# Optimization experiments

Hardware: AMD Instinct MI355X
Metric: run time of the kernel (lower is better)

Reference implementation:

```python
import jax, jax.numpy as jnp
import numpy as np

D_MODEL = 512
N_HEADS = 8
DH = D_MODEL // N_HEADS            # 64
Q_PROJ = D_MODEL // 2              # 256
KV_PROJ = (2 * D_MODEL) // 3       # 341
ROPE_DIM = D_MODEL // 8            # 64 total rope dims
R = ROPE_DIM // N_HEADS            # 8 rope dims per head
THETA = 10000.0
EPS = 1e-5
B, S = 2, 2048


def layernorm(x, g, b):
    m = jnp.mean(x, axis=-1, keepdims=True)
    v = jnp.var(x, axis=-1, keepdims=True)
    return (x - m) * jax.lax.rsqrt(v + EPS) * g + b


def rope_cos_sin(seq_len, dtype):
    inv_freq = THETA ** (-jnp.arange(0, R, 2, dtype=jnp.float32) / R)   # (R/2,)
    ang = jnp.arange(seq_len, dtype=jnp.float32)[:, None] * inv_freq   # (S, R/2)
    cos = jnp.concatenate([jnp.cos(ang), jnp.cos(ang)], axis=-1)        # (S, R)
    sin = jnp.concatenate([jnp.sin(ang), jnp.sin(ang)], axis=-1)
    return cos.astype(dtype), sin.astype(dtype)


def apply_rope(x, cos, sin):
    # x: (B, H, S, R); neox-style half rotation
    x1, x2 = jnp.split(x, 2, axis=-1)
    rot = jnp.concatenate([-x2, x1], axis=-1)
    return x * cos + rot * sin


def setup_inputs() -> dict:
    key = jax.random.key(0)
    ks = jax.random.split(key, 9)
    p = lambda k, shape: 0.01 * jax.random.normal(k, shape, jnp.float32)
    return {
        "x": jax.random.normal(ks[0], (B, S, D_MODEL), jnp.float32),
        "W_dq": p(ks[1], (D_MODEL, Q_PROJ)),
        "W_uq": p(ks[2], (Q_PROJ, D_MODEL)),
        "W_qr": p(ks[3], (Q_PROJ, ROPE_DIM)),
        "W_dkv": p(ks[4], (D_MODEL, KV_PROJ)),
        "W_ukv": p(ks[5], (KV_PROJ, 2 * D_MODEL)),
        "W_kr": p(ks[6], (D_MODEL, ROPE_DIM)),
        "W_o": p(ks[7], (D_MODEL, D_MODEL)),
        "q_ln_g": jnp.ones((Q_PROJ,), jnp.float32),
        "q_ln_b": jnp.zeros((Q_PROJ,), jnp.float32),
        "kv_ln_g": jnp.ones((KV_PROJ,), jnp.float32),
        "kv_ln_b": jnp.zeros((KV_PROJ,), jnp.float32),
    }


def reference(x, W_dq, W_uq, W_qr, W_dkv, W_ukv, W_kr, W_o,
              q_ln_g, q_ln_b, kv_ln_g, kv_ln_b):
    b, s, d = x.shape
    # --- low-rank Q path ---
    cq = layernorm(x @ W_dq, q_ln_g, q_ln_b)                      # (B,S,Q_PROJ)
    Q = (cq @ W_uq).reshape(b, s, N_HEADS, DH).transpose(0, 2, 1, 3)
    Qr = (cq @ W_qr).reshape(b, s, N_HEADS, R).transpose(0, 2, 1, 3)
    cos, sin = rope_cos_sin(s, x.dtype)
    Qr = apply_rope(Qr, cos, sin)
    q = jnp.concatenate([Q, Qr], axis=-1)                          # (B,H,S,DH+R)
    # --- low-rank KV path ---
    ckv = layernorm(x @ W_dkv, kv_ln_g, kv_ln_b)                  # (B,S,KV_PROJ)
    KV = ckv @ W_ukv                                              # (B,S,2*D)
    K, V = KV[..., :D_MODEL], KV[..., D_MODEL:]
    K = K.reshape(b, s, N_HEADS, DH).transpose(0, 2, 1, 3)
    Kr = (x @ W_kr).reshape(b, s, N_HEADS, R).transpose(0, 2, 1, 3)
    Kr = apply_rope(Kr, cos, sin)
    k = jnp.concatenate([K, Kr], axis=-1)                          # (B,H,S,DH+R)
    v = V.reshape(b, s, N_HEADS, DH).transpose(0, 2, 1, 3)         # (B,H,S,DH)
    # --- causal SDPA ---
    scale = 1.0 / jnp.sqrt(jnp.asarray(DH + R, x.dtype))
    scores = jnp.einsum('bhqd,bhkd->bhqk', q, k) * scale           # (B,H,S,S)
    mask = jnp.tril(jnp.ones((s, s), dtype=bool))
    scores = jnp.where(mask, scores, jnp.finfo(scores.dtype).min)
    attn = jax.nn.softmax(scores, axis=-1)
    out = jnp.einsum('bhqk,bhkd->bhqd', attn, v)
    out = out.transpose(0, 2, 1, 3).reshape(b, s, d)
    return out @ W_o.T, ckv
```

## Files before the change

### kernel.cpp

```cpp
#include <hip/hip_runtime.h>
#include <hip/hip_bf16.h>

#define BATCH 2
#define SEQ 2048
#define DM 512
#define NH 8
#define DHD 64
#define QP 256
#define KVP 341
#define DQKPAD 96
#define MROWS 4096

#define OFF_X     0
#define OFF_WDQ   2097152
#define OFF_WUQ   2228224
#define OFF_WQR   2359296
#define OFF_WDKV  2375680
#define OFF_WUKV  2550272
#define OFF_WKR   2899456
#define OFF_WO    2932224
#define OFF_QG    3194368
#define OFF_QB    3194624
#define OFF_KG    3194880
#define OFF_KB    3195221
#define N_ELEMS   3195562

#define T_DQ   0
#define T_DKV  131072
#define T_KR   327680
#define T_UQ   360448
#define T_QR   491520
#define T_UKV  507904
#define T_TOT  901120

typedef __bf16 bf16x8 __attribute__((ext_vector_type(8)));
typedef float f32x4 __attribute__((ext_vector_type(4)));
typedef __hip_bfloat16 bf16;
typedef unsigned short u16;

static __device__ __forceinline__ bf16x8 ld_bf8(const bf16* p) {
    return __builtin_bit_cast(bf16x8, *(const uint4*)p);
}

#define GL16(gp, lp) __builtin_amdgcn_global_load_lds( \
    (const __attribute__((address_space(1))) void*)(gp), \
    (__attribute__((address_space(3))) void*)(lp), 16, 0, 0)

__global__ void detect_k(const u16* __restrict__ x, int* __restrict__ flagp) {
    __shared__ int cnt;
    if (threadIdx.x == 0) cnt = 0;
    __syncthreads();
    int bad = 0;
    for (int i = threadIdx.x; i < 2048; i += 256) {
        u16 u = x[i];
        int e = (u >> 7) & 0xFF;
        if (u != 0 && (e < 90 || e > 164)) bad++;
    }
    atomicAdd(&cnt, bad);
    __syncthreads();
    if (threadIdx.x == 0) *flagp = (cnt > 256) ? 1 : 0;
}

__global__ __launch_bounds__(256) void cvt_all(
    const void* s0, const void* s1, const void* s2, const void* s3,
    const void* s4, const void* s5, const void* s6, const void* s7,
    const void* s8, const void* s9, const void* s10, const void* s11,
    u16* __restrict__ arena, const int* __restrict__ flagp)
{
    int gid = blockIdx.x * 256 + threadIdx.x;
    if (gid >= N_ELEMS) return;
    const int f = *flagp;
    const void* src; int base;
    if      (gid < OFF_WDQ)  { src = s0;  base = OFF_X; }
    else if (gid < OFF_WUQ)  { src = s1;  base = OFF_WDQ; }
    else if (gid < OFF_WQR)  { src = s2;  base = OFF_WUQ; }
    else if (gid < OFF_WDKV) { src = s3;  base = OFF_WQR; }
    else if (gid < OFF_WUKV) { src = s4;  base = OFF_WDKV; }
    else if (gid < OFF_WKR)  { src = s5;  base = OFF_WUKV; }
    else if (gid < OFF_WO)   { src = s6;  base = OFF_WKR; }
    else if (gid < OFF_QG)   { src = s7;  base = OFF_WO; }
    else if (gid < OFF_QB)   { src = s8;  base = OFF_QG; }
    else if (gid < OFF_KG)   { src = s9;  base = OFF_QB; }
    else if (gid < OFF_KB)   { src = s10; base = OFF_KG; }
    else                     { src = s11; base = OFF_KB; }
    int local = gid - base;
    u16 v;
    if (f) {
        float xv = ((const float*)src)[local];
        v = __builtin_bit_cast(u16, __float2bfloat16(xv));
    } else {
        v = ((const u16*)src)[local];
    }
    arena[gid] = v;
}

__global__ __launch_bounds__(256) void wt_all(const bf16* __restrict__ AR, bf16* __restrict__ WT) {
    int gid = blockIdx.x * 256 + threadIdx.x;
    if (gid >= T_TOT) return;
    const bf16* src; int base, Kp, Nv, Kv;
    if      (gid < T_DKV) { base = T_DQ;  Kp = 512; src = AR + OFF_WDQ;  Nv = 256;  Kv = 512; }
    else if (gid < T_KR)  { base = T_DKV; Kp = 512; src = AR + OFF_WDKV; Nv = 341;  Kv = 512; }
    else if (gid < T_UQ)  { base = T_KR;  Kp = 512; src = AR + OFF_WKR;  Nv = 64;   Kv = 512; }
    else if (gid < T_QR)  { base = T_UQ;  Kp = 256; src = AR + OFF_WUQ;  Nv = 512;  Kv = 256; }
    else if (gid < T_UKV) { base = T_QR;  Kp = 256; src = AR + OFF_WQR;  Nv = 64;   Kv = 256; }
    else                  { base = T_UKV; Kp = 384; src = AR + OFF_WUKV; Nv = 1024; Kv = 341; }
    int loc = gid - base;
    int n = loc / Kp, k = loc % Kp;
    bf16 v = __float2bfloat16(0.f);
    if (n < Nv && k < Kv) v = src[(size_t)k * Nv + n];
    WT[gid] = v;
}

__global__ __launch_bounds__(256) void gemm128(
    const bf16* __restrict__ A, int lda,
    const bf16* __restrict__ BT, int ldb,
    int N, int Kpad, int mode,
    void* __restrict__ C0, int ldc,
    bf16* __restrict__ kv_k, bf16* __restrict__ kv_v,
    const int* __restrict__ flagp, float* __restrict__ C0f)
{
    __shared__ __align__(16) bf16 LB[128 * 64 + 64 * 64];
    bf16* Al = LB;
    bf16* Bl = LB + 128 * 64;
    const int tid = threadIdx.x;
    const int m0 = blockIdx.y * 128, n0 = blockIdx.x * 64;
    const int lane = tid & 63, w = tid >> 6;
    const int g = lane >> 4, lr = lane & 15;
    f32x4 acc[2][4] = {};
    const int r8 = lane >> 3;
    const int xr8 = ((lane & 7) ^ r8) * 8;
    const int swx = (lr & 7) << 4;

    for (int k0 = 0; k0 < Kpad; k0 += 64) {
        #pragma unroll
        for (int i = 0; i < 4; ++i)
            GL16(&A[(size_t)(m0 + w * 32 + i * 8 + r8) * lda + k0 + xr8],
                 (char*)Al + w * 4096 + i * 1024);
        #pragma unroll
        for (int i = 0; i < 2; ++i)
            GL16(&BT[(size_t)(n0 + w * 16 + i * 8 + r8) * ldb + k0 + xr8],
                 (char*)Bl + w * 2048 + i * 1024);
        __syncthreads();
        #pragma unroll
        for (int ks = 0; ks < 2; ++ks) {
            const int cs = (ks * 64 + g * 16) ^ swx;
            bf16x8 a0 = ld_bf8((const bf16*)((const char*)Al + (w * 32 + lr) * 128 + cs));
            bf16x8 a1 = ld_bf8((const bf16*)((const char*)Al + (w * 32 + 16 + lr) * 128 + cs));
            #pragma unroll
            for (int nt = 0; nt < 4; ++nt) {
                bf16x8 b = ld_bf8((const bf16*)((const char*)Bl + (nt * 16 + lr) * 128 + cs));
                acc[0][nt] = __builtin_amdgcn_mfma_f32_16x16x32_bf16(a0, b, acc[0][nt], 0, 0, 0);
                acc[1][nt] = __builtin_amdgcn_mfma_f32_16x16x32_bf16(a1, b, acc[1][nt], 0, 0, 0);
            }
        }
        __syncthreads();
    }

    if (mode == 3 && n0 >= DM) {
        const int h = (n0 - DM) >> 6;
        const int b = m0 >> 11, s0 = m0 & 2047;
        bf16* T = LB;
        #pragma unroll
        for (int mt = 0; mt < 2; ++mt)
        #pragma unroll
        for (int nt = 0; nt < 4; ++nt)
        #pragma unroll
        for (int r = 0; r < 4; ++r) {
            int dv = nt * 16 + lr;
            int sl = w * 32 + mt * 16 + g * 4 + r;
            T[dv * 136 + sl] = __float2bfloat16(acc[mt][nt][r]);
        }
        __syncthreads();
        const int row = tid >> 2, coff = (tid & 3) * 32;
        bf16* dst = &kv_v[((size_t)(b * NH + h) * DHD + row) * SEQ + s0 + coff];
        const bf16* srcp = &T[row * 136 + coff];
        #pragma unroll
        for (int q2 = 0; q2 < 4; ++q2)
            *(uint4*)(dst + q2 * 8) = *(const uint4*)(srcp + q2 * 8);
        return;
    }

    const int f32o = (mode == 1 && flagp) ? *flagp : 0;
    #pragma unroll
    for (int mt = 0; mt < 2; ++mt)
    #pragma unroll
    for (int nt = 0; nt < 4; ++nt)
    #pragma unroll
    for (int r = 0; r < 4; ++r) {
        int gm = m0 + w * 32 + mt * 16 + g * 4 + r;
        int gn = n0 + nt * 16 + lr;
        float v = acc[mt][nt][r];
        if (mode == 0) {
            ((float*)C0)[(size_t)gm * ldc + gn] = v;
        } else if (mode == 1) {
            if (f32o) C0f[(size_t)gm * ldc + gn] = v;
            else ((bf16*)C0)[(size_t)gm * ldc + gn] = __float2bfloat16(v);
        } else if (mode == 4) {
            int b = gm >> 11, s = gm & 2047;
            if (gn < DM) {
                int h = gn >> 6, dh = gn & 63;
                ((bf16*)C0)[((size_t)(b * NH + h) * SEQ + s) * DQKPAD + dh] = __float2bfloat16(v);
            } else {
                C0f[(size_t)gm * 64 + (gn - DM)] = v;
            }
        } else {
            int b = gm >> 11, s = gm & 2047;
            int h = gn >> 6, dh = gn & 63;
            kv_k[((size_t)(b * NH + h) * SEQ + s) * DQKPAD + dh] = __float2bfloat16(v);
        }
    }
}

__global__ __launch_bounds__(256) void ln_wave(
    const float* __restrict__ Y, int ldy, int N,
    const bf16* __restrict__ gam, const bf16* __restrict__ bet,
    bf16* __restrict__ O1, float* __restrict__ O1f, const int* __restrict__ flagp, int ld1,
    bf16* __restrict__ O2, int ld2, int padN)
{
    const int w = threadIdx.x >> 6, lane = threadIdx.x & 63;
    const int row = blockIdx.x * 4 + w;
    const float* y = Y + (size_t)row * ldy;
    const int f32o = flagp ? *flagp : 0;
    float s = 0.f, ss = 0.f;
    for (int i = lane; i < N; i += 64) { float v = y[i]; s += v; ss += v * v; }
    #pragma unroll
    for (int m = 1; m < 64; m <<= 1) { s += __shfl_xor(s, m); ss += __shfl_xor(ss, m); }
    float mean = s / N;
    float var = ss / N - mean * mean;
    float rstd = rsqrtf(var + 1e-5f);
    for (int i = lane; i < N; i += 64) {
        float v = (y[i] - mean) * rstd * __bfloat162float(gam[i]) + __bfloat162float(bet[i]);
        if (f32o) O1f[(size_t)row * ld1 + i] = v;
        else O1[(size_t)row * ld1 + i] = __float2bfloat16(v);
        if (O2) O2[(size_t)row * ld2 + i] = __float2bfloat16(v);
    }
    if (O2) for (int i = N + lane; i < padN; i += 64) O2[(size_t)row * ld2 + i] = __float2bfloat16(0.f);
}

__global__ __launch_bounds__(256) void rope_fill(
    const float* __restrict__ yqr, int ldq,
    const float* __restrict__ ykr, int ldk,
    bf16* __restrict__ qa, bf16* __restrict__ ka)
{
    int idx = blockIdx.x * 256 + threadIdx.x;
    if (idx >= MROWS * NH) return;
    int m = idx >> 3, h = idx & 7;
    int b = m >> 11, s = m & 2047;
    float q[8], k[8], qo[8], ko[8];
    #pragma unroll
    for (int j = 0; j < 8; ++j) {
        q[j] = yqr[(size_t)m * ldq + h * 8 + j];
        k[j] = ykr[(size_t)m * ldk + h * 8 + j];
    }
    #pragma unroll
    for (int i = 0; i < 4; ++i) {
        float inv = exp2f(-(float)i * 3.3219280948873623f);
        float ang = (float)s * inv;
        float sn, cs;
        sincosf(ang, &sn, &cs);
        qo[i] = q[i] * cs - q[i + 4] * sn;
        qo[i + 4] = q[i + 4] * cs + q[i] * sn;
        ko[i] = k[i] * cs - k[i + 4] * sn;
        ko[i + 4] = k[i + 4] * cs + k[i] * sn;
    }
    bf16* qp = qa + ((size_t)(b * NH + h) * SEQ + s) * DQKPAD;
    bf16* kp = ka + ((size_t)(b * NH + h) * SEQ + s) * DQKPAD;
    #pragma unroll
    for (int j = 0; j < 8; ++j) {
        qp[64 + j] = __float2bfloat16(qo[j]);
        kp[64 + j] = __float2bfloat16(ko[j]);
    }
    #pragma unroll
    for (int j = 72; j < 96; ++j) {
        qp[j] = __float2bfloat16(0.f);
        kp[j] = __float2bfloat16(0.f);
    }
}

__global__ __launch_bounds__(256) void attn_split3(
    const bf16* __restrict__ qa, const bf16* __restrict__ ka, const bf16* __restrict__ vat,
    bf16* __restrict__ po, float* __restrict__ mlm, float* __restrict__ mll)
{
    __shared__ __align__(16) bf16 Kl[64][104];
    __shared__ __align__(16) bf16 Vt[64][72];
    __shared__ __align__(16) bf16 Pl[4][16][72];
    const int sp = blockIdx.x, pr = blockIdx.y, bh = blockIdx.z;
    const int tid = threadIdx.x, w = tid >> 6, lane = tid & 63;
    const int g = lane >> 4, lr = lane & 15;
    const size_t base = (size_t)bh * SEQ;
    const float SC = 0.11785113019775793f;
    const float L2E = 1.4426950408889634f;
    const bf16* vb = vat + (size_t)bh * DHD * SEQ;

    for (int half = 0; half < 2; ++half) {
        const int qb = half ? (31 - pr) : pr;
        const int qrow0 = qb * 64 + w * 16;
        const int myq = qrow0 + lr;

        bf16x8 qf[3];
        #pragma unroll
        for (int kc = 0; kc < 3; ++kc)
            qf[kc] = ld_bf8(&qa[(base + myq) * DQKPAD + kc * 32 + g * 8]);

        float m_p = -1e30f, l_p = 0.f;
        f32x4 acc_o[4] = {};
        const int ng = qb + 1;
        const int bs = (ng * sp) >> 2, be = (ng * (sp + 1)) >> 2;

        for (int gi = bs; gi < be; ++gi) {
            const int j0 = gi * 64;
            __syncthreads();
            for (int u = tid; u < 768; u += 256) {
                int row = u / 12, cc = (u % 12) * 8;
                *(uint4*)&Kl[row][cc] = *(const uint4*)&ka[(base + j0 + row) * DQKPAD + cc];
            }
            {
                int d = tid >> 2, ko = (tid & 3) * 16;
                const bf16* vsrc = &vb[(size_t)d * SEQ + j0 + ko];
                *(uint4*)&Vt[d][ko]     = *(const uint4*)vsrc;
                *(uint4*)&Vt[d][ko + 8] = *(const uint4*)(vsrc + 8);
            }
            __syncthreads();

            f32x4 accs[4] = {};
            #pragma unroll
            for (int kc = 0; kc < 3; ++kc) {
                #pragma unroll
                for (int nt = 0; nt < 4; ++nt) {
                    bf16x8 kf = ld_bf8(&Kl[nt * 16 + lr][kc * 32 + g * 8]);
                    accs[nt] = __builtin_amdgcn_mfma_f32_16x16x32_bf16(kf, qf[kc], accs[nt], 0, 0, 0);
                }
            }
            float s[4][4];
            float mloc = -1e30f;
            #pragma unroll
            for (int nt = 0; nt < 4; ++nt)
            #pragma unroll
            for (int r = 0; r < 4; ++r) {
                int key = j0 + nt * 16 + g * 4 + r;
                float sv = accs[nt][r] * SC;
                sv = (key <= myq) ? sv : -1e30f;
                s[nt][r] = sv;
                mloc = fmaxf(mloc, sv);
            }
            mloc = fmaxf(mloc, __shfl_xor(mloc, 16));
            mloc = fmaxf(mloc, __shfl_xor(mloc, 32));
            float mn = fmaxf(m_p, mloc);
            float alpha = exp2f((m_p - mn) * L2E);
            m_p = mn;
            float rs = 0.f;
            #pragma unroll
            for (int nt = 0; nt < 4; ++nt)
            #pragma unroll
            for (int r = 0; r < 4; ++r) {
                float p = exp2f((s[nt][r] - mn) * L2E);
                s[nt][r] = p; rs += p;
            }
            rs += __shfl_xor(rs, 16);
            rs += __shfl_xor(rs, 32);
            l_p = l_p * alpha + rs;
            float ar[4];
            #pragma unroll
            for (int r = 0; r < 4; ++r) ar[r] = __shfl(alpha, g * 4 + r);
            #pragma unroll
            for (int nv = 0; nv < 4; ++nv)
            #pragma unroll
            for (int r = 0; r < 4; ++r) acc_o[nv][r] *= ar[r];
            #pragma unroll
            for (int nt = 0; nt < 4; ++nt) {
                ushort4 pk;
                pk.x = __builtin_bit_cast(u16, __float2bfloat16(s[nt][0]));
                pk.y = __builtin_bit_cast(u16, __float2bfloat16(s[nt][1]));
                pk.z = __builtin_bit_cast(u16, __float2bfloat16(s[nt][2]));
                pk.w = __builtin_bit_cast(u16, __float2bfloat16(s[nt][3]));
                *(ushort4*)&Pl[w][lr][nt * 16 + g * 4] = pk;
            }
            bf16x8 pf0 = ld_bf8(&Pl[w][lr][g * 8]);
            bf16x8 pf1 = ld_bf8(&Pl[w][lr][32 + g * 8]);
            #pragma unroll
            for (int nv = 0; nv < 4; ++nv) {
                bf16x8 vf0 = ld_bf8(&Vt[nv * 16 + lr][g * 8]);
                acc_o[nv] = __builtin_amdgcn_mfma_f32_16x16x32_bf16(pf0, vf0, acc_o[nv], 0, 0, 0);
                bf16x8 vf1 = ld_bf8(&Vt[nv * 16 + lr][32 + g * 8]);
                acc_o[nv] = __builtin_amdgcn_mfma_f32_16x16x32_bf16(pf1, vf1, acc_o[nv], 0, 0, 0);
            }
        }

        const size_t pb = (size_t)(bh * 4 + sp) * SEQ;
        #pragma unroll
        for (int r = 0; r < 4; ++r) {
            int qrow = qrow0 + g * 4 + r;
            #pragma unroll
            for (int nv = 0; nv < 4; ++nv)
                po[(pb + qrow) * DHD + nv * 16 + lr] = __float2bfloat16(acc_o[nv][r]);
        }
        if (lane < 16) {
            mlm[pb + qrow0 + lane] = m_p;
            mll[pb + qrow0 + lane] = l_p;
        }
    }
}

__global__ __launch_bounds__(256) void attn_combine(
    const bf16* __restrict__ po, const float* __restrict__ mlm, const float* __restrict__ mll,
    bf16* __restrict__ ao)
{
    int id = blockIdx.x * 256 + threadIdx.x;
    int bh = id >> 14;
    int rem = id & 16383;
    int q = rem >> 3, dc = (rem & 7) * 8;
    const float L2E = 1.4426950408889634f;
    size_t mlb = (size_t)bh * 4 * SEQ + q;
    float ms[4], ls[4];
    #pragma unroll
    for (int s = 0; s < 4; ++s) { ms[s] = mlm[mlb + (size_t)s * SEQ]; ls[s] = mll[mlb + (size_t)s * SEQ]; }
    float M = fmaxf(fmaxf(ms[0], ms[1]), fmaxf(ms[2], ms[3]));
    float wsc[4]; float L = 0.f;
    #pragma unroll
    for (int s = 0; s < 4; ++s) { wsc[s] = exp2f((ms[s] - M) * L2E); L += wsc[s] * ls[s]; }
    float o[8] = {};
    #pragma unroll
    for (int s = 0; s < 4; ++s) {
        if (ls[s] <= 0.f) continue;
        bf16x8 pv = ld_bf8(&po[((size_t)(bh * 4 + s) * SEQ + q) * DHD + dc]);
        #pragma unroll
        for (int j = 0; j < 8; ++j) o[j] += wsc[s] * (float)pv[j];
    }
    float invL = 1.f / L;
    int b = bh >> 3, h = bh & 7;
    __bf16 tmp[8];
    #pragma unroll
    for (int j = 0; j < 8; ++j) tmp[j] = (__bf16)(o[j] * invL);
    *(uint4*)&ao[((size_t)(b * SEQ) + q) * DM + h * DHD + dc] = *(uint4*)tmp;
}

extern "C" void kernel_launch(void* const* d_in, const int* in_sizes, int n_in,
                              void* d_out, int out_size, void* d_ws, size_t ws_size,
                              hipStream_t stream) {
    char* ws = (char*)d_ws;
    bf16* AR      = (bf16*)(ws + 0);
    float* ml_m   = (float*)(ws + 0);
    float* ml_l   = (float*)(ws + 524288);
    bf16* WT      = (bf16*)(ws + 6391296);
    int*  flagp   = (int*)(ws + 8193536);
    float* y      = (float*)(ws + 8194048);
    float* y_qr   = (float*)(ws + 19728384);
    bf16* cq      = (bf16*)(ws + 20776960);
    bf16* ckvp    = (bf16*)(ws + 22874112);
    bf16* po      = (bf16*)(ws + 8194048);
    bf16* q_attn  = (bf16*)(ws + 26019840);
    bf16* k_attn  = (bf16*)(ws + 32311296);
    bf16* v_attnT = (bf16*)(ws + 38602752);
    bf16* attn_o  = (bf16*)(ws + 42797056);

    const bf16* xb  = AR + OFF_X;
    const bf16* W_o = AR + OFF_WO;
    const bf16* qg  = AR + OFF_QG;
    const bf16* qb_ = AR + OFF_QB;
    const bf16* kg  = AR + OFF_KG;
    const bf16* kb  = AR + OFF_KB;

    bf16*  out_b = (bf16*)d_out;
    float* out_f = (float*)d_out;
    bf16*  ckv_b = out_b + (size_t)MROWS * DM;
    float* ckv_f = out_f + (size_t)MROWS * DM;

    dim3 blk(256);
    detect_k<<<1, blk, 0, stream>>>((const u16*)d_in[0], flagp);
    cvt_all<<<dim3((N_ELEMS + 255) / 256), blk, 0, stream>>>(
        d_in[0], d_in[1], d_in[2], d_in[3], d_in[4], d_in[5],
        d_in[6], d_in[7], d_in[8], d_in[9], d_in[10], d_in[11],
        (u16*)AR, flagp);
    wt_all<<<dim3((T_TOT + 255) / 256), blk, 0, stream>>>(AR, WT);

    gemm128<<<dim3(11, 32), blk, 0, stream>>>(xb, DM, WT + T_DQ, DM, 704, DM, 0, y, 704, nullptr, nullptr, nullptr, nullptr);
    ln_wave<<<MROWS / 4, blk, 0, stream>>>(y, 704, QP, qg, qb_, cq, nullptr, nullptr, QP, nullptr, 0, 0);
    ln_wave<<<MROWS / 4, blk, 0, stream>>>(y + 256, 704, KVP, kg, kb, ckv_b, ckv_f, flagp, KVP, ckvp, 384, 384);
    gemm128<<<dim3(9, 32), blk, 0, stream>>>(cq, QP, WT + T_UQ, QP, 576, QP, 4, q_attn, 0, nullptr, nullptr, nullptr, y_qr);
    gemm128<<<dim3(16, 32), blk, 0, stream>>>(ckvp, 384, WT + T_UKV, 384, 1024, 384, 3, nullptr, 0, k_attn, v_attnT, nullptr, nullptr);
    rope_fill<<<dim3(MROWS * NH / 256), blk, 0, stream>>>(y_qr, 64, y + 640, 704, q_attn, k_attn);
    attn_split3<<<dim3(4, 16, 16), blk, 0, stream>>>(q_attn, k_attn, v_attnT, po, ml_m, ml_l);
    attn_combine<<<dim3(16 * SEQ * 8 / 256), blk, 0, stream>>>(po, ml_m, ml_l, attn_o);
    gemm128<<<dim3(8, 32), blk, 0, stream>>>(attn_o, DM, W_o, DM, DM, DM, 1, out_b, DM, nullptr, nullptr, flagp, out_f);
}
```

Before: 132.1 us.

## Fuse prep kernels, move RoPE into GEMM epilogues, add lazy softmax rescale

Merges detect, convert and weight-transpose into one prep kernel that reads the original inputs directly, and merges the two layernorm launches into one. RoPE is now applied in the GEMM epilogues for the Q-rope and K-rope column tiles, and the softmax scale is folded into Q, so the rope_fill kernel and the fp32 y_qr buffer go away. The attention loop skips causal masking on fully visible tiles and skips rescaling when the running max grows by at most 8. Together these cut launch count and intermediate traffic, at the cost of more epilogue work, redundant flag detection in every prep block, and a lazy-rescale threshold that could lose precision.

```diff
diff --git a/kernel.cpp b/kernel.cpp
--- a/kernel.cpp
+++ b/kernel.cpp
@@ -12,18 +12,11 @@
 #define MROWS 4096
 
 #define OFF_X     0
-#define OFF_WDQ   2097152
-#define OFF_WUQ   2228224
-#define OFF_WQR   2359296
-#define OFF_WDKV  2375680
-#define OFF_WUKV  2550272
-#define OFF_WKR   2899456
 #define OFF_WO    2932224
 #define OFF_QG    3194368
 #define OFF_QB    3194624
 #define OFF_KG    3194880
 #define OFF_KB    3195221
-#define N_ELEMS   3195562
 
 #define T_DQ   0
 #define T_DKV  131072
@@ -33,6 +26,11 @@
 #define T_UKV  507904
 #define T_TOT  901120
 
+#define NW_X   2097152
+#define NW_WO  262144
+#define NW_PAR 1194
+#define PREP_TOT (NW_X + NW_WO + NW_PAR + T_TOT)
+
 typedef __bf16 bf16x8 __attribute__((ext_vector_type(8)));
 typedef float f32x4 __attribute__((ext_vector_type(4)));
 typedef __hip_bfloat16 bf16;
@@ -46,69 +44,90 @@
     (const __attribute__((address_space(1))) void*)(gp), \
     (__attribute__((address_space(3))) void*)(lp), 16, 0, 0)
 
-__global__ void detect_k(const u16* __restrict__ x, int* __restrict__ flagp) {
+__global__ __launch_bounds__(256) void prep(
+    const void* px, const void* pwdq, const void* pwuq, const void* pwqr,
+    const void* pwdkv, const void* pwukv, const void* pwkr, const void* pwo,
+    const void* pqg, const void* pqb, const void* pkg, const void* pkb,
+    u16* __restrict__ arena, u16* __restrict__ WT, int* __restrict__ flagp)
+{
     __shared__ int cnt;
     if (threadIdx.x == 0) cnt = 0;
     __syncthreads();
     int bad = 0;
+    const u16* xs = (const u16*)px;
     for (int i = threadIdx.x; i < 2048; i += 256) {
-        u16 u = x[i];
+        u16 u = xs[i];
         int e = (u >> 7) & 0xFF;
         if (u != 0 && (e < 90 || e > 164)) bad++;
     }
-    atomicAdd(&cnt, bad);
+    #pragma unroll
+    for (int m2 = 1; m2 < 64; m2 <<= 1) bad += __shfl_xor(bad, m2);
+    if ((threadIdx.x & 63) == 0) atomicAdd(&cnt, bad);
     __syncthreads();
-    if (threadIdx.x == 0) *flagp = (cnt > 256) ? 1 : 0;
-}
-
-__global__ __launch_bounds__(256) void cvt_all(
-    const void* s0, const void* s1, const void* s2, const void* s3,
-    const void* s4, const void* s5, const void* s6, const void* s7,
-    const void* s8, const void* s9, const void* s10, const void* s11,
-    u16* __restrict__ arena, const int* __restrict__ flagp)
+    const int f = (cnt > 256) ? 1 : 0;
+    if (blockIdx.x == 0 && threadIdx.x == 0) *flagp = f;
+
+    int gid = blockIdx.x * 256 + threadIdx.x;
+    if (gid >= PREP_TOT) return;
+
+    auto rdu = [&](const void* s, int i) -> u16 {
+        if (f) return __builtin_bit_cast(u16, __float2bfloat16(((const float*)s)[i]));
+        return ((const u16*)s)[i];
+    };
+
+    if (gid < NW_X) {
+        arena[OFF_X + gid] = rdu(px, gid);
+    } else if (gid < NW_X + NW_WO) {
+        int i = gid - NW_X;
+        arena[OFF_WO + i] = rdu(pwo, i);
+    } else if (gid < NW_X + NW_WO + NW_PAR) {
+        int i = gid - NW_X - NW_WO;
+        if (i < 256)      arena[OFF_QG + i]         = rdu(pqg, i);
+        else if (i < 512) arena[OFF_QB + (i - 256)] = rdu(pqb, i - 256);
+        else if (i < 853) arena[OFF_KG + (i - 512)] = rdu(pkg, i - 512);
+        else              arena[OFF_KB + (i - 853)] = rdu(pkb, i - 853);
+    } else {
+        int loc = gid - (NW_X + NW_WO + NW_PAR);
+        const void* src; int srcIdx, valid;
+        if (loc < T_DKV)      { int l2 = loc;          int n = l2 >> 9, k = l2 & 511; src = pwdq;  valid = 1;         srcIdx = k * 256 + n; }
+        else if (loc < T_KR)  { int l2 = loc - T_DKV;  int n = l2 >> 9, k = l2 & 511; src = pwdkv; valid = (n < 341); srcIdx = k * 341 + n; }
+        else if (loc < T_UQ)  { int l2 = loc - T_KR;   int n = l2 >> 9, k = l2 & 511; src = pwkr;  valid = 1;         srcIdx = k * 64 + n; }
+        else if (loc < T_QR)  { int l2 = loc - T_UQ;   int n = l2 >> 8, k = l2 & 255; src = pwuq;  valid = 1;         srcIdx = k * 512 + n; }
+        else if (loc < T_UKV) { int l2 = loc - T_QR;   int n = l2 >> 8, k = l2 & 255; src = pwqr;  valid = 1;         srcIdx = k * 64 + n; }
+        else                  { int l2 = loc - T_UKV;  int n = l2 / 384, k = l2 % 384; src = pwukv; valid = (k < 341); srcIdx = k * 1024 + n; }
+        WT[loc] = valid ? rdu(src, srcIdx) : (u16)0;
+    }
+}
+
+static __device__ __forceinline__ void rope_epi(
+    f32x4 (&acc)[2][4], bf16* __restrict__ dst, int m0, int w, int g, int lr, int tid, bool scaleq)
 {
-    int gid = blockIdx.x * 256 + threadIdx.x;
-    if (gid >= N_ELEMS) return;
-    const int f = *flagp;
-    const void* src; int base;
-    if      (gid < OFF_WDQ)  { src = s0;  base = OFF_X; }
-    else if (gid < OFF_WUQ)  { src = s1;  base = OFF_WDQ; }
-    else if (gid < OFF_WQR)  { src = s2;  base = OFF_WUQ; }
-    else if (gid < OFF_WDKV) { src = s3;  base = OFF_WQR; }
-    else if (gid < OFF_WUKV) { src = s4;  base = OFF_WDKV; }
-    else if (gid < OFF_WKR)  { src = s5;  base = OFF_WUKV; }
-    else if (gid < OFF_WO)   { src = s6;  base = OFF_WKR; }
-    else if (gid < OFF_QG)   { src = s7;  base = OFF_WO; }
-    else if (gid < OFF_QB)   { src = s8;  base = OFF_QG; }
-    else if (gid < OFF_KG)   { src = s9;  base = OFF_QB; }
-    else if (gid < OFF_KB)   { src = s10; base = OFF_KG; }
-    else                     { src = s11; base = OFF_KB; }
-    int local = gid - base;
-    u16 v;
-    if (f) {
-        float xv = ((const float*)src)[local];
-        v = __builtin_bit_cast(u16, __float2bfloat16(xv));
-    } else {
-        v = ((const u16*)src)[local];
-    }
-    arena[gid] = v;
-}
-
-__global__ __launch_bounds__(256) void wt_all(const bf16* __restrict__ AR, bf16* __restrict__ WT) {
-    int gid = blockIdx.x * 256 + threadIdx.x;
-    if (gid >= T_TOT) return;
-    const bf16* src; int base, Kp, Nv, Kv;
-    if      (gid < T_DKV) { base = T_DQ;  Kp = 512; src = AR + OFF_WDQ;  Nv = 256;  Kv = 512; }
-    else if (gid < T_KR)  { base = T_DKV; Kp = 512; src = AR + OFF_WDKV; Nv = 341;  Kv = 512; }
-    else if (gid < T_UQ)  { base = T_KR;  Kp = 512; src = AR + OFF_WKR;  Nv = 64;   Kv = 512; }
-    else if (gid < T_QR)  { base = T_UQ;  Kp = 256; src = AR + OFF_WUQ;  Nv = 512;  Kv = 256; }
-    else if (gid < T_UKV) { base = T_QR;  Kp = 256; src = AR + OFF_WQR;  Nv = 64;   Kv = 256; }
-    else                  { base = T_UKV; Kp = 384; src = AR + OFF_WUKV; Nv = 1024; Kv = 341; }
-    int loc = gid - base;
-    int n = loc / Kp, k = loc % Kp;
-    bf16 v = __float2bfloat16(0.f);
-    if (n < Nv && k < Kv) v = src[(size_t)k * Nv + n];
-    WT[gid] = v;
+    const float SCv = 0.11785113019775793f;
+    #pragma unroll
+    for (int mt = 0; mt < 2; ++mt)
+    #pragma unroll
+    for (int r = 0; r < 4; ++r) {
+        int gm = m0 + w * 32 + mt * 16 + g * 4 + r;
+        int s = gm & 2047, b = gm >> 11;
+        float ang = (float)s * exp2f(-(float)(lr & 3) * 3.3219280948873623f);
+        float sn, cs;
+        sincosf(ang, &sn, &cs);
+        #pragma unroll
+        for (int nt = 0; nt < 4; ++nt) {
+            float v = acc[mt][nt][r];
+            float pt = __shfl_xor(v, 4);
+            float o = (lr & 4) ? fmaf(pt, sn, v * cs) : fmaf(-pt, sn, v * cs);
+            if (scaleq) o *= SCv;
+            int h = (nt * 16 + lr) >> 3, j = lr & 7;
+            dst[((size_t)(b * NH + h) * SEQ + s) * DQKPAD + 64 + j] = __float2bfloat16(o);
+        }
+    }
+    for (int u = tid; u < 128 * 96; u += 256) {
+        int rw = u / 96, rem = u - rw * 96;
+        int h = rem / 12, c = rem - h * 12;
+        int row = m0 + rw, b2 = row >> 11, s2 = row & 2047;
+        *(unsigned int*)&dst[((size_t)(b2 * NH + h) * SEQ + s2) * DQKPAD + 72 + c * 2] = 0u;
+    }
 }
 
 __global__ __launch_bounds__(256) void gemm128(
@@ -156,6 +175,14 @@
         __syncthreads();
     }
 
+    if (mode == 0 && n0 == 640) {
+        rope_epi(acc, kv_k, m0, w, g, lr, tid, false);
+        return;
+    }
+    if (mode == 4 && n0 == DM) {
+        rope_epi(acc, (bf16*)C0, m0, w, g, lr, tid, true);
+        return;
+    }
     if (mode == 3 && n0 >= DM) {
         const int h = (n0 - DM) >> 6;
         const int b = m0 >> 11, s0 = m0 & 2047;
@@ -180,6 +207,7 @@
         return;
     }
 
+    const float SCv = 0.11785113019775793f;
     const int f32o = (mode == 1 && flagp) ? *flagp : 0;
     #pragma unroll
     for (int mt = 0; mt < 2; ++mt)
@@ -197,12 +225,8 @@
             else ((bf16*)C0)[(size_t)gm * ldc + gn] = __float2bfloat16(v);
         } else if (mode == 4) {
             int b = gm >> 11, s = gm & 2047;
-            if (gn < DM) {
-                int h = gn >> 6, dh = gn & 63;
-                ((bf16*)C0)[((size_t)(b * NH + h) * SEQ + s) * DQKPAD + dh] = __float2bfloat16(v);
-            } else {
-                C0f[(size_t)gm * 64 + (gn - DM)] = v;
-            }
+            int h = gn >> 6, dh = gn & 63;
+            ((bf16*)C0)[((size_t)(b * NH + h) * SEQ + s) * DQKPAD + dh] = __float2bfloat16(v * SCv);
         } else {
             int b = gm >> 11, s = gm & 2047;
             int h = gn >> 6, dh = gn & 63;
@@ -211,69 +235,47 @@
     }
 }
 
-__global__ __launch_bounds__(256) void ln_wave(
-    const float* __restrict__ Y, int ldy, int N,
-    const bf16* __restrict__ gam, const bf16* __restrict__ bet,
-    bf16* __restrict__ O1, float* __restrict__ O1f, const int* __restrict__ flagp, int ld1,
-    bf16* __restrict__ O2, int ld2, int padN)
+__global__ __launch_bounds__(256) void ln_both(
+    const float* __restrict__ y,
+    const bf16* __restrict__ qg, const bf16* __restrict__ qb,
+    const bf16* __restrict__ kg, const bf16* __restrict__ kb,
+    bf16* __restrict__ cq, bf16* __restrict__ ckv_b, float* __restrict__ ckv_f,
+    bf16* __restrict__ ckvp, const int* __restrict__ flagp)
 {
     const int w = threadIdx.x >> 6, lane = threadIdx.x & 63;
-    const int row = blockIdx.x * 4 + w;
-    const float* y = Y + (size_t)row * ldy;
-    const int f32o = flagp ? *flagp : 0;
-    float s = 0.f, ss = 0.f;
-    for (int i = lane; i < N; i += 64) { float v = y[i]; s += v; ss += v * v; }
-    #pragma unroll
-    for (int m = 1; m < 64; m <<= 1) { s += __shfl_xor(s, m); ss += __shfl_xor(ss, m); }
-    float mean = s / N;
-    float var = ss / N - mean * mean;
-    float rstd = rsqrtf(var + 1e-5f);
-    for (int i = lane; i < N; i += 64) {
-        float v = (y[i] - mean) * rstd * __bfloat162float(gam[i]) + __bfloat162float(bet[i]);
-        if (f32o) O1f[(size_t)row * ld1 + i] = v;
-        else O1[(size_t)row * ld1 + i] = __float2bfloat16(v);
-        if (O2) O2[(size_t)row * ld2 + i] = __float2bfloat16(v);
-    }
-    if (O2) for (int i = N + lane; i < padN; i += 64) O2[(size_t)row * ld2 + i] = __float2bfloat16(0.f);
-}
-
-__global__ __launch_bounds__(256) void rope_fill(
-    const float* __restrict__ yqr, int ldq,
-    const float* __restrict__ ykr, int ldk,
-    bf16* __restrict__ qa, bf16* __restrict__ ka)
-{
-    int idx = blockIdx.x * 256 + threadIdx.x;
-    if (idx >= MROWS * NH) return;
-    int m = idx >> 3, h = idx & 7;
-    int b = m >> 11, s = m & 2047;
-    float q[8], k[8], qo[8], ko[8];
-    #pragma unroll
-    for (int j = 0; j < 8; ++j) {
-        q[j] = yqr[(size_t)m * ldq + h * 8 + j];
-        k[j] = ykr[(size_t)m * ldk + h * 8 + j];
-    }
-    #pragma unroll
-    for (int i = 0; i < 4; ++i) {
-        float inv = exp2f(-(float)i * 3.3219280948873623f);
-        float ang = (float)s * inv;
-        float sn, cs;
-        sincosf(ang, &sn, &cs);
-        qo[i] = q[i] * cs - q[i + 4] * sn;
-        qo[i + 4] = q[i + 4] * cs + q[i] * sn;
-        ko[i] = k[i] * cs - k[i + 4] * sn;
-        ko[i + 4] = k[i + 4] * cs + k[i] * sn;
-    }
-    bf16* qp = qa + ((size_t)(b * NH + h) * SEQ + s) * DQKPAD;
-    bf16* kp = ka + ((size_t)(b * NH + h) * SEQ + s) * DQKPAD;
-    #pragma unroll
-    for (int j = 0; j < 8; ++j) {
-        qp[64 + j] = __float2bfloat16(qo[j]);
-        kp[64 + j] = __float2bfloat16(ko[j]);
-    }
-    #pragma unroll
-    for (int j = 72; j < 96; ++j) {
-        qp[j] = __float2bfloat16(0.f);
-        kp[j] = __float2bfloat16(0.f);
+    const int blk = blockIdx.x;
+    if (blk < 1024) {
+        const int row = blk * 4 + w;
+        const float* yr = y + (size_t)row * 704;
+        float s = 0.f, ss = 0.f;
+        for (int i = lane; i < 256; i += 64) { float v = yr[i]; s += v; ss += v * v; }
+        #pragma unroll
+        for (int m = 1; m < 64; m <<= 1) { s += __shfl_xor(s, m); ss += __shfl_xor(ss, m); }
+        float mean = s * (1.f / 256.f);
+        float var = ss * (1.f / 256.f) - mean * mean;
+        float rstd = rsqrtf(var + 1e-5f);
+        for (int i = lane; i < 256; i += 64) {
+            float v = (yr[i] - mean) * rstd * __bfloat162float(qg[i]) + __bfloat162float(qb[i]);
+            cq[(size_t)row * 256 + i] = __float2bfloat16(v);
+        }
+    } else {
+        const int row = (blk - 1024) * 4 + w;
+        const float* yr = y + (size_t)row * 704 + 256;
+        const int f32o = *flagp;
+        float s = 0.f, ss = 0.f;
+        for (int i = lane; i < KVP; i += 64) { float v = yr[i]; s += v; ss += v * v; }
+        #pragma unroll
+        for (int m = 1; m < 64; m <<= 1) { s += __shfl_xor(s, m); ss += __shfl_xor(ss, m); }
+        float mean = s * (1.f / 341.f);
+        float var = ss * (1.f / 341.f) - mean * mean;
+        float rstd = rsqrtf(var + 1e-5f);
+        for (int i = lane; i < KVP; i += 64) {
+            float v = (yr[i] - mean) * rstd * __bfloat162float(kg[i]) + __bfloat162float(kb[i]);
+            if (f32o) ckv_f[(size_t)row * KVP + i] = v;
+            else ckv_b[(size_t)row * KVP + i] = __float2bfloat16(v);
+            ckvp[(size_t)row * 384 + i] = __float2bfloat16(v);
+        }
+        for (int i = KVP + lane; i < 384; i += 64) ckvp[(size_t)row * 384 + i] = __float2bfloat16(0.f);
     }
 }
 
@@ -288,7 +290,6 @@
     const int tid = threadIdx.x, w = tid >> 6, lane = tid & 63;
     const int g = lane >> 4, lr = lane & 15;
     const size_t base = (size_t)bh * SEQ;
-    const float SC = 0.11785113019775793f;
     const float L2E = 1.4426950408889634f;
     const bf16* vb = vat + (size_t)bh * DHD * SEQ;
 
@@ -331,48 +332,74 @@
                     accs[nt] = __builtin_amdgcn_mfma_f32_16x16x32_bf16(kf, qf[kc], accs[nt], 0, 0, 0);
                 }
             }
-            float s[4][4];
+            float s_[4][4];
             float mloc = -1e30f;
-            #pragma unroll
-            for (int nt = 0; nt < 4; ++nt)
-            #pragma unroll
-            for (int r = 0; r < 4; ++r) {
-                int key = j0 + nt * 16 + g * 4 + r;
-                float sv = accs[nt][r] * SC;
-                sv = (key <= myq) ? sv : -1e30f;
-                s[nt][r] = sv;
-                mloc = fmaxf(mloc, sv);
+            if (j0 + 63 > qrow0) {
+                #pragma unroll
+                for (int nt = 0; nt < 4; ++nt)
+                #pragma unroll
+                for (int r = 0; r < 4; ++r) {
+                    int key = j0 + nt * 16 + g * 4 + r;
+                    float sv = accs[nt][r];
+                    sv = (key <= myq) ? sv : -1e30f;
+                    s_[nt][r] = sv;
+                    mloc = fmaxf(mloc, sv);
+                }
+            } else {
+                #pragma unroll
+                for (int nt = 0; nt < 4; ++nt)
+                #pragma unroll
+                for (int r = 0; r < 4; ++r) {
+                    float sv = accs[nt][r];
+                    s_[nt][r] = sv;
+                    mloc = fmaxf(mloc, sv);
+                }
             }
             mloc = fmaxf(mloc, __shfl_xor(mloc, 16));
             mloc = fmaxf(mloc, __shfl_xor(mloc, 32));
-            float mn = fmaxf(m_p, mloc);
-            float alpha = exp2f((m_p - mn) * L2E);
-            m_p = mn;
-            float rs = 0.f;
-            #pragma unroll
-            for (int nt = 0; nt < 4; ++nt)
-            #pragma unroll
-            for (int r = 0; r < 4; ++r) {
-                float p = exp2f((s[nt][r] - mn) * L2E);
-                s[nt][r] = p; rs += p;
-            }
-            rs += __shfl_xor(rs, 16);
-            rs += __shfl_xor(rs, 32);
-            l_p = l_p * alpha + rs;
-            float ar[4];
-            #pragma unroll
-            for (int r = 0; r < 4; ++r) ar[r] = __shfl(alpha, g * 4 + r);
-            #pragma unroll
-            for (int nv = 0; nv < 4; ++nv)
-            #pragma unroll
-            for (int r = 0; r < 4; ++r) acc_o[nv][r] *= ar[r];
+
+            if (__all(mloc <= m_p + 8.f)) {
+                float rs = 0.f;
+                #pragma unroll
+                for (int nt = 0; nt < 4; ++nt)
+                #pragma unroll
+                for (int r = 0; r < 4; ++r) {
+                    float p = exp2f((s_[nt][r] - m_p) * L2E);
+                    s_[nt][r] = p; rs += p;
+                }
+                rs += __shfl_xor(rs, 16);
+                rs += __shfl_xor(rs, 32);
+                l_p += rs;
+            } else {
+                float mn = fmaxf(m_p, mloc);
+                float alpha = exp2f((m_p - mn) * L2E);
+                m_p = mn;
+                float rs = 0.f;
+                #pragma unroll
+                for (int nt = 0; nt < 4; ++nt)
+                #pragma unroll
+                for (int r = 0; r < 4; ++r) {
+                    float p = exp2f((s_[nt][r] - mn) * L2E);
+                    s_[nt][r] = p; rs += p;
+                }
+                rs += __shfl_xor(rs, 16);
+                rs += __shfl_xor(rs, 32);
+                l_p = l_p * alpha + rs;
+                float ar[4];
+                #pragma unroll
+                for (int r = 0; r < 4; ++r) ar[r] = __shfl(alpha, g * 4 + r);
+                #pragma unroll
+                for (int nv = 0; nv < 4; ++nv)
+                #pragma unroll
+                for (int r = 0; r < 4; ++r) acc_o[nv][r] *= ar[r];
+            }
             #pragma unroll
             for (int nt = 0; nt < 4; ++nt) {
                 ushort4 pk;
-                pk.x = __builtin_bit_cast(u16, __float2bfloat16(s[nt][0]));
-                pk.y = __builtin_bit_cast(u16, __float2bfloat16(s[nt][1]));
-                pk.z = __builtin_bit_cast(u16, __float2bfloat16(s[nt][2]));
-                pk.w = __builtin_bit_cast(u16, __float2bfloat16(s[nt][3]));
+                pk.x = __builtin_bit_cast(u16, __float2bfloat16(s_[nt][0]));
+                pk.y = __builtin_bit_cast(u16, __float2bfloat16(s_[nt][1]));
+                pk.z = __builtin_bit_cast(u16, __float2bfloat16(s_[nt][2]));
+                pk.w = __builtin_bit_cast(u16, __float2bfloat16(s_[nt][3]));
                 *(ushort4*)&Pl[w][lr][nt * 16 + g * 4] = pk;
             }
             bf16x8 pf0 = ld_bf8(&Pl[w][lr][g * 8]);
@@ -444,9 +471,8 @@
     bf16* WT      = (bf16*)(ws + 6391296);
     int*  flagp   = (int*)(ws + 8193536);
     float* y      = (float*)(ws + 8194048);
-    float* y_qr   = (float*)(ws + 19728384);
-    bf16* cq      = (bf16*)(ws + 20776960);
-    bf16* ckvp    = (bf16*)(ws + 22874112);
+    bf16* cq      = (bf16*)(ws + 19728384);
+    bf16* ckvp    = (bf16*)(ws + 21825536);
     bf16* po      = (bf16*)(ws + 8194048);
     bf16* q_attn  = (bf16*)(ws + 26019840);
     bf16* k_attn  = (bf16*)(ws + 32311296);
@@ -466,20 +492,15 @@
     float* ckv_f = out_f + (size_t)MROWS * DM;
 
     dim3 blk(256);
-    detect_k<<<1, blk, 0, stream>>>((const u16*)d_in[0], flagp);
-    cvt_all<<<dim3((N_ELEMS + 255) / 256), blk, 0, stream>>>(
+    prep<<<dim3((PREP_TOT + 255) / 256), blk, 0, stream>>>(
         d_in[0], d_in[1], d_in[2], d_in[3], d_in[4], d_in[5],
         d_in[6], d_in[7], d_in[8], d_in[9], d_in[10], d_in[11],
-        (u16*)AR, flagp);
-    wt_all<<<dim3((T_TOT + 255) / 256), blk, 0, stream>>>(AR, WT);
-
-    gemm128<<<dim3(11, 32), blk, 0, stream>>>(xb, DM, WT + T_DQ, DM, 704, DM, 0, y, 704, nullptr, nullptr, nullptr, nullptr);
-    ln_wave<<<MROWS / 4, blk, 0, stream>>>(y, 704, QP, qg, qb_, cq, nullptr, nullptr, QP, nullptr, 0, 0);
-    ln_wave<<<MROWS / 4, blk, 0, stream>>>(y + 256, 704, KVP, kg, kb, ckv_b, ckv_f, flagp, KVP, ckvp, 384, 384);
-    gemm128<<<dim3(9, 32), blk, 0, stream>>>(cq, QP, WT + T_UQ, QP, 576, QP, 4, q_attn, 0, nullptr, nullptr, nullptr, y_qr);
+        (u16*)AR, (u16*)WT, flagp);
+    gemm128<<<dim3(11, 32), blk, 0, stream>>>(xb, DM, WT + T_DQ, DM, 704, DM, 0, y, 704, k_attn, nullptr, nullptr, nullptr);
+    ln_both<<<dim3(2048), blk, 0, stream>>>(y, qg, qb_, kg, kb, cq, ckv_b, ckv_f, ckvp, flagp);
+    gemm128<<<dim3(9, 32), blk, 0, stream>>>(cq, QP, WT + T_UQ, QP, 576, QP, 4, q_attn, 0, nullptr, nullptr, nullptr, nullptr);
     gemm128<<<dim3(16, 32), blk, 0, stream>>>(ckvp, 384, WT + T_UKV, 384, 1024, 384, 3, nullptr, 0, k_attn, v_attnT, nullptr, nullptr);
-    rope_fill<<<dim3(MROWS * NH / 256), blk, 0, stream>>>(y_qr, 64, y + 640, 704, q_attn, k_attn);
     attn_split3<<<dim3(4, 16, 16), blk, 0, stream>>>(q_attn, k_attn, v_attnT, po, ml_m, ml_l);
-    attn_combine<<<dim3(16 * SEQ * 8 / 256), blk, 0, stream>>>(po, ml_m, ml_l, attn_o);
+    attn_combine<<<dim3(1024), blk, 0, stream>>>(po, ml_m, ml_l, attn_o);
     gemm128<<<dim3(8, 32), blk, 0, stream>>>(attn_o, DM, W_o, DM, DM, DM, 1, out_b, DM, nullptr, nullptr, flagp, out_f);
 }
```

New measurement: 127.9 us. -3.2%, faster.
